# Kernel tuning notes

Hardware: AMD Instinct MI355X
Metric: run time of the kernel (lower is better)

Reference implementation:

```python
import jax, jax.numpy as jnp
import numpy as np

MIN_POS = 1e-6
EPS = 1e-20
B, S, F_IN, E, H = 2, 1024, 768, 768, 12
DH = E // H   # nnmf in_features per head (64)
FH = E // H   # nnmf out_features per head (hidden_features=embed_dim default)
N_NNMF_ITERS = 3
N_ALPHA_ITERS = 3


def l1norm(x, axis=-1):
    # F.normalize(x, p=1, dim=axis, eps=1e-20) for non-negative x
    return x / jnp.maximum(jnp.sum(jnp.abs(x), axis=axis, keepdims=True), EPS)


def setup_inputs() -> dict:
    key = jax.random.key(0)
    k = jax.random.split(key, 6)
    return {
        "x": jax.random.normal(k[0], (B, S, F_IN), jnp.float32),
        "embed_w": jax.random.normal(k[1], (E, F_IN), jnp.float32) * 0.02,
        "embed_b": jnp.zeros((E,), jnp.float32),
        "nnmf_w": jax.random.uniform(k[2], (FH, DH), jnp.float32),  # non-negative NMF dictionary
        "out_w": jax.random.normal(k[3], (F_IN, E), jnp.float32) * 0.02,
        "out_b": jnp.zeros((F_IN,), jnp.float32),
    }


def reference(x, embed_w, embed_b, nnmf_w, out_w, out_b):
    # normalize NMF weight rows (p=1 over in_features), as nnmf_layer.normalize_weights
    W = nnmf_w / jnp.maximum(jnp.sum(nnmf_w, axis=1, keepdims=True), EPS)  # [FH, DH]

    # embed + clamp positive, split heads
    xe = jnp.clip(x @ embed_w.T + embed_b, MIN_POS)            # [B,S,E]
    xe = xe.reshape(B, S, H, DH)                                # [B,S,H,DH]

    # NNMFDense: prepared_input = l1-normalized input (normalize_input_dim=-1)
    inp = l1norm(xe)                                            # [B,S,H,DH]
    h = l1norm(jnp.ones((B, S, H, FH), x.dtype))                # init hidden
    rec = inp
    for _ in range(N_NNMF_ITERS):
        rec = l1norm(jnp.clip(h @ W, MIN_POS))                  # reconstruction [B,S,H,DH]
        h = l1norm(jnp.clip(h * ((inp / rec) @ W.T), MIN_POS))  # multiplicative update

    # normalize_h (p=1, dim=-1)
    h = l1norm(h)                                               # [B,S,H,FH] -> 'bohf'

    # alpha dynamics fixed point
    alpha = jnp.ones((B, H, S, S), x.dtype)                     # 'bhoi'
    h_rec_input = rec * inp                                     # [B,S,H,DH]
    for _ in range(N_ALPHA_ITERS):
        h_mixed = jnp.einsum('bohf,bhoi->bihf', h, alpha)       # [B,S,H,FH]
        arec_inv = 1.0 / (h_mixed @ W + EPS)                    # _reconstruct -> [B,S,H,DH]
        alpha = alpha * jnp.einsum('bohf,bihf->bhoi', h_rec_input, arec_inv)

    out = jnp.einsum('bohf,bhoi->bihf', h, alpha)               # [B,S,H,FH]
    out = out.reshape(B, S, E)                                  # flatten heads
    return out @ out_w.T + out_b                                # out_project
```

## Files before the change

kernel.cpp:

```cpp
#include <hip/hip_runtime.h>

#define B_  2
#define S_  1024
#define FIN 768
#define E_  768
#define H_  12
#define DH  64

typedef unsigned int uint;
typedef unsigned short ushort;
typedef __attribute__((ext_vector_type(8))) short short8;
typedef __attribute__((ext_vector_type(4))) float floatx4;

__device__ __forceinline__ ushort f2bf(float f) {
    uint u = __float_as_uint(f);
    return (ushort)((u + 0x7fffu + ((u >> 16) & 1u)) >> 16);
}

__device__ __forceinline__ uint4 pack8(const ushort* p) {
    uint4 r;
    r.x = (uint)p[0] | ((uint)p[1] << 16);
    r.y = (uint)p[2] | ((uint)p[3] << 16);
    r.z = (uint)p[4] | ((uint)p[5] << 16);
    r.w = (uint)p[6] | ((uint)p[7] << 16);
    return r;
}

__device__ __forceinline__ void split8v(float4 a, float4 b, short8& hi, short8& lo) {
    float v[8] = {a.x, a.y, a.z, a.w, b.x, b.y, b.z, b.w};
    ushort h[8], l[8];
#pragma unroll
    for (int j = 0; j < 8; ++j) {
        h[j] = f2bf(v[j]);
        l[j] = f2bf(v[j] - __uint_as_float(((uint)h[j]) << 16));
    }
    uint4 H = pack8(h), L = pack8(l);
    hi = *(short8*)&H;
    lo = *(short8*)&L;
}

__global__ __launch_bounds__(256) void k_embed_prep(const float* __restrict__ xs,
                                                    const float* __restrict__ ew,
                                                    const float* __restrict__ eb,
                                                    const float* __restrict__ nw,
                                                    float* __restrict__ Wn,
                                                    float* __restrict__ WnT,
                                                    float* __restrict__ r1inv,
                                                    float* __restrict__ zbase,
                                                    float* __restrict__ inp) {
    __shared__ __align__(16) unsigned char smem[28160];
    const int tid = threadIdx.x;
    const int bid = blockIdx.x;

    if (bid >= 768) {
        const int pb = bid - 768;
        if (pb == 0) {
            float* Wl = (float*)smem;
            const int f = tid >> 2, q = tid & 3;
            float v[16];
            float s = 0.f;
#pragma unroll
            for (int i = 0; i < 16; ++i) { v[i] = nw[f * 64 + q * 16 + i]; s += v[i]; }
            s += __shfl_xor(s, 1, 64);
            s += __shfl_xor(s, 2, 64);
            const float inv = 1.f / fmaxf(s, 1e-20f);
#pragma unroll
            for (int i = 0; i < 16; ++i) {
                float w = v[i] * inv;
                Wn[f * 64 + q * 16 + i] = w;
                WnT[(q * 16 + i) * 64 + f] = w;
                Wl[f * 65 + q * 16 + i] = w;
            }
            __syncthreads();
            if (tid < 64) {
                float cs = 0.f;
                for (int ff = 0; ff < 64; ++ff) cs += Wl[ff * 65 + tid];
                float t = fmaxf(cs * (1.f / 64.f), 1e-6f);
                float S = t;
#pragma unroll
                for (int m = 1; m < 64; m <<= 1) S += __shfl_xor(S, m, 64);
                S = fmaxf(S, 1e-20f);
                r1inv[tid] = S / t;
            }
        } else {
            const int i = (pb - 1) * 1024 + tid * 4;
            if (i < 26112) {
                float4 z = make_float4(0.f, 0.f, 0.f, 0.f);
                *(float4*)(zbase + i) = z;
            }
        }
        return;
    }

    const int head = bid % 12;
    const int tok0 = (bid / 12) * 32;
    ushort* As_hi = (ushort*)smem;
    ushort* As_lo = As_hi + 32 * 72;
    ushort* Bs_hi = As_lo + 32 * 72;
    ushort* Bs_lo = Bs_hi + 64 * 72;
    float*  RS    = (float*)(Bs_lo + 64 * 72);

    const int wv = tid >> 6, lane = tid & 63;
    const int mbase = (wv >> 1) * 16;
    const int nbase = (wv & 1) * 32;
    const int lm = lane & 15, lq = lane >> 4;

    floatx4 acc[2];
    acc[0] = (floatx4)0.f;
    acc[1] = (floatx4)0.f;

    const int arow = tid >> 3, akc = (tid & 7) * 8;
    const int brow = tid >> 2, bkq = (tid & 3) * 16;
    const float* xrow = xs + (size_t)(tok0 + arow) * FIN + akc;
    const float* wrg  = ew + (size_t)(head * 64 + brow) * FIN + bkq;

    float4 pa[2], pb[4];
#pragma unroll
    for (int c = 0; c < 2; ++c) pa[c] = *(const float4*)(xrow + c * 4);
#pragma unroll
    for (int c = 0; c < 4; ++c) pb[c] = *(const float4*)(wrg + c * 4);

    for (int kb = 0; kb < FIN; kb += 64) {
        __syncthreads();
        {
            ushort ah[8], al[8], bh[16], bl[16];
            float va[8] = {pa[0].x, pa[0].y, pa[0].z, pa[0].w,
                           pa[1].x, pa[1].y, pa[1].z, pa[1].w};
#pragma unroll
            for (int j = 0; j < 8; ++j) {
                ah[j] = f2bf(va[j]);
                al[j] = f2bf(va[j] - __uint_as_float(((uint)ah[j]) << 16));
            }
#pragma unroll
            for (int c4 = 0; c4 < 4; ++c4) {
                float vb[4] = {pb[c4].x, pb[c4].y, pb[c4].z, pb[c4].w};
#pragma unroll
                for (int j = 0; j < 4; ++j) {
                    ushort g = f2bf(vb[j]);
                    bh[c4 * 4 + j] = g;
                    bl[c4 * 4 + j] = f2bf(vb[j] - __uint_as_float(((uint)g) << 16));
                }
            }
            const int aoff = arow * 72 + akc;
            *(uint4*)&As_hi[aoff] = pack8(ah);
            *(uint4*)&As_lo[aoff] = pack8(al);
            const int boff = brow * 72 + bkq;
            *(uint4*)&Bs_hi[boff]     = pack8(bh);
            *(uint4*)&Bs_hi[boff + 8] = pack8(bh + 8);
            *(uint4*)&Bs_lo[boff]     = pack8(bl);
            *(uint4*)&Bs_lo[boff + 8] = pack8(bl + 8);
        }
        __syncthreads();
        if (kb + 64 < FIN) {
#pragma unroll
            for (int c = 0; c < 2; ++c) pa[c] = *(const float4*)(xrow + kb + 64 + c * 4);
#pragma unroll
            for (int c = 0; c < 4; ++c) pb[c] = *(const float4*)(wrg + kb + 64 + c * 4);
        }
#pragma unroll
        for (int ch = 0; ch < 2; ++ch) {
            const int ko = ch * 32 + lq * 8;
            short8 ah = *(const short8*)&As_hi[(mbase + lm) * 72 + ko];
            short8 al = *(const short8*)&As_lo[(mbase + lm) * 72 + ko];
#pragma unroll
            for (int ti = 0; ti < 2; ++ti) {
                short8 bh = *(const short8*)&Bs_hi[(nbase + ti * 16 + lm) * 72 + ko];
                short8 bl = *(const short8*)&Bs_lo[(nbase + ti * 16 + lm) * 72 + ko];
                acc[ti] = __builtin_amdgcn_mfma_f32_16x16x32_bf16(ah, bh, acc[ti], 0, 0, 0);
                acc[ti] = __builtin_amdgcn_mfma_f32_16x16x32_bf16(al, bh, acc[ti], 0, 0, 0);
                acc[ti] = __builtin_amdgcn_mfma_f32_16x16x32_bf16(ah, bl, acc[ti], 0, 0, 0);
            }
        }
    }

    const float b0 = eb[head * 64 + nbase + lm];
    const float b1 = eb[head * 64 + nbase + 16 + lm];
    float xe[2][4];
    float rs[4];
#pragma unroll
    for (int r = 0; r < 4; ++r) {
        float e0 = fmaxf(acc[0][r] + b0, 1e-6f);
        float e1 = fmaxf(acc[1][r] + b1, 1e-6f);
        xe[0][r] = e0; xe[1][r] = e1;
        float p = e0 + e1;
        p += __shfl_xor(p, 1, 64);
        p += __shfl_xor(p, 2, 64);
        p += __shfl_xor(p, 4, 64);
        p += __shfl_xor(p, 8, 64);
        rs[r] = p;
    }
    if (lm == 0) {
#pragma unroll
        for (int r = 0; r < 4; ++r)
            RS[(wv & 1) * 32 + mbase + lq * 4 + r] = rs[r];
    }
    __syncthreads();
    const size_t obase = ((size_t)((tok0 >> 10) * 12 + head) * 1024 + (tok0 & 1023));
#pragma unroll
    for (int r = 0; r < 4; ++r) {
        const int m = mbase + lq * 4 + r;
        const float inv = 1.f / fmaxf(RS[m] + RS[32 + m], 1e-20f);
        float* op = inp + (obase + m) * 64;
        op[nbase + lm]      = xe[0][r] * inv;
        op[nbase + 16 + lm] = xe[1][r] * inv;
    }
}

__device__ __forceinline__ void mfma_matvec(const float srcC[4][4], float* T,
                                            int lm, int lq,
                                            const short8 Bh[4][2],
                                            const short8 Bl[4][2],
                                            floatx4 out[4]) {
#pragma unroll
    for (int nt = 0; nt < 4; ++nt)
#pragma unroll
        for (int r = 0; r < 4; ++r)
            T[(lq * 4 + r) * 68 + nt * 16 + lm] = srcC[nt][r];
    __syncthreads();
    float4 a00 = *(const float4*)&T[lm * 68 + lq * 8];
    float4 a01 = *(const float4*)&T[lm * 68 + lq * 8 + 4];
    float4 a10 = *(const float4*)&T[lm * 68 + 32 + lq * 8];
    float4 a11 = *(const float4*)&T[lm * 68 + 32 + lq * 8 + 4];
    short8 A0h, A0l, A1h, A1l;
    split8v(a00, a01, A0h, A0l);
    split8v(a10, a11, A1h, A1l);
#pragma unroll
    for (int nt = 0; nt < 4; ++nt) {
        floatx4 acc = (floatx4)0.f;
        acc = __builtin_amdgcn_mfma_f32_16x16x32_bf16(A0h, Bh[nt][0], acc, 0, 0, 0);
        acc = __builtin_amdgcn_mfma_f32_16x16x32_bf16(A0l, Bh[nt][0], acc, 0, 0, 0);
        acc = __builtin_amdgcn_mfma_f32_16x16x32_bf16(A0h, Bl[nt][0], acc, 0, 0, 0);
        acc = __builtin_amdgcn_mfma_f32_16x16x32_bf16(A1h, Bh[nt][1], acc, 0, 0, 0);
        acc = __builtin_amdgcn_mfma_f32_16x16x32_bf16(A1l, Bh[nt][1], acc, 0, 0, 0);
        acc = __builtin_amdgcn_mfma_f32_16x16x32_bf16(A1h, Bl[nt][1], acc, 0, 0, 0);
        out[nt] = acc;
    }
}

__global__ __launch_bounds__(256) void k_nnmf(const float* __restrict__ inp,
                                              const float* __restrict__ Wn,
                                              const float* __restrict__ WnT,
                                              const float* __restrict__ r1inv,
                                              float* __restrict__ hout,
                                              float* __restrict__ hriout,
                                              float* __restrict__ mp0) {
    __shared__ float Tb[4][16 * 68];
    const int tid = threadIdx.x, wv = tid >> 6, lane = tid & 63;
    const int lm = lane & 15, lq = lane >> 4;
    float* T = Tb[wv];
    const int rowbase = blockIdx.x * 64 + wv * 16;

    short8 Bt_h[4][2], Bt_l[4][2], Bw_h[4][2], Bw_l[4][2];
#pragma unroll
    for (int nt = 0; nt < 4; ++nt)
#pragma unroll
        for (int kc = 0; kc < 2; ++kc) {
            const int idx = (nt * 16 + lm) * 64 + kc * 32 + lq * 8;
            split8v(*(const float4*)(WnT + idx), *(const float4*)(WnT + idx + 4),
                    Bt_h[nt][kc], Bt_l[nt][kc]);
            split8v(*(const float4*)(Wn + idx), *(const float4*)(Wn + idx + 4),
                    Bw_h[nt][kc], Bw_l[nt][kc]);
        }

    float inpC[4][4];
#pragma unroll
    for (int nt = 0; nt < 4; ++nt)
#pragma unroll
        for (int r = 0; r < 4; ++r)
            inpC[nt][r] = inp[(size_t)(rowbase + lq * 4 + r) * 64 + nt * 16 + lm];
    float r1c[4];
#pragma unroll
    for (int nt = 0; nt < 4; ++nt) r1c[nt] = r1inv[nt * 16 + lm];

    float hC[4][4], recC[4][4];
    {
        float qC[4][4];
#pragma unroll
        for (int nt = 0; nt < 4; ++nt)
#pragma unroll
            for (int r = 0; r < 4; ++r) qC[nt][r] = inpC[nt][r] * r1c[nt];
        floatx4 u[4];
        mfma_matvec(qC, T, lm, lq, Bw_h, Bw_l, u);
#pragma unroll
        for (int nt = 0; nt < 4; ++nt)
#pragma unroll
            for (int r = 0; r < 4; ++r)
                hC[nt][r] = fmaxf(u[nt][r] * (1.f / 64.f), 1e-6f);
#pragma unroll
        for (int r = 0; r < 4; ++r) {
            float s = (hC[0][r] + hC[1][r]) + (hC[2][r] + hC[3][r]);
            s += __shfl_xor(s, 1, 64); s += __shfl_xor(s, 2, 64);
            s += __shfl_xor(s, 4, 64); s += __shfl_xor(s, 8, 64);
            const float inv = __builtin_amdgcn_rcpf(fmaxf(s, 1e-20f));
#pragma unroll
            for (int nt = 0; nt < 4; ++nt) hC[nt][r] *= inv;
        }
    }
#pragma unroll 1
    for (int it = 0; it < 2; ++it) {
        floatx4 t[4];
        mfma_matvec(hC, T, lm, lq, Bt_h, Bt_l, t);
        float tC[4][4], qC[4][4];
#pragma unroll
        for (int nt = 0; nt < 4; ++nt)
#pragma unroll
            for (int r = 0; r < 4; ++r) tC[nt][r] = fmaxf(t[nt][r], 1e-6f);
#pragma unroll
        for (int r = 0; r < 4; ++r) {
            float s = (tC[0][r] + tC[1][r]) + (tC[2][r] + tC[3][r]);
            s += __shfl_xor(s, 1, 64); s += __shfl_xor(s, 2, 64);
            s += __shfl_xor(s, 4, 64); s += __shfl_xor(s, 8, 64);
            s = fmaxf(s, 1e-20f);
            const float invS = __builtin_amdgcn_rcpf(s);
#pragma unroll
            for (int nt = 0; nt < 4; ++nt) {
                recC[nt][r] = tC[nt][r] * invS;
                qC[nt][r] = inpC[nt][r] * s * __builtin_amdgcn_rcpf(tC[nt][r]);
            }
        }
        floatx4 u[4];
        mfma_matvec(qC, T, lm, lq, Bw_h, Bw_l, u);
#pragma unroll
        for (int nt = 0; nt < 4; ++nt)
#pragma unroll
            for (int r = 0; r < 4; ++r)
                hC[nt][r] = fmaxf(hC[nt][r] * u[nt][r], 1e-6f);
#pragma unroll
        for (int r = 0; r < 4; ++r) {
            float s = (hC[0][r] + hC[1][r]) + (hC[2][r] + hC[3][r]);
            s += __shfl_xor(s, 1, 64); s += __shfl_xor(s, 2, 64);
            s += __shfl_xor(s, 4, 64); s += __shfl_xor(s, 8, 64);
            const float inv = __builtin_amdgcn_rcpf(fmaxf(s, 1e-20f));
#pragma unroll
            for (int nt = 0; nt < 4; ++nt) hC[nt][r] *= inv;
        }
    }
#pragma unroll
    for (int r = 0; r < 4; ++r) {
        float s = (hC[0][r] + hC[1][r]) + (hC[2][r] + hC[3][r]);
        s += __shfl_xor(s, 1, 64); s += __shfl_xor(s, 2, 64);
        s += __shfl_xor(s, 4, 64); s += __shfl_xor(s, 8, 64);
        const float inv = __builtin_amdgcn_rcpf(fmaxf(s, 1e-20f));
#pragma unroll
        for (int nt = 0; nt < 4; ++nt) hC[nt][r] *= inv;
    }
#pragma unroll
    for (int nt = 0; nt < 4; ++nt)
#pragma unroll
        for (int r = 0; r < 4; ++r) {
            const size_t o = (size_t)(rowbase + lq * 4 + r) * 64 + nt * 16 + lm;
            hout[o] = hC[nt][r];
            hriout[o] = recC[nt][r] * inpC[nt][r];
        }
    float hs[4];
#pragma unroll
    for (int nt = 0; nt < 4; ++nt) {
        float s = (hC[nt][0] + hC[nt][1]) + (hC[nt][2] + hC[nt][3]);
        s += __shfl_xor(s, 16, 64);
        s += __shfl_xor(s, 32, 64);
        hs[nt] = s;
    }
    float mvv = lq == 0 ? hs[0] : lq == 1 ? hs[1] : lq == 2 ? hs[2] : hs[3];
    atomicAdd(&mp0[(size_t)blockIdx.x * 64 + lq * 16 + lm], mvv);
}

__global__ __launch_bounds__(256) void k_alpha_step(const float* __restrict__ hin,
                                                    const float* __restrict__ hri,
                                                    const float* __restrict__ Wn,
                                                    const float* __restrict__ mp_in,
                                                    float* __restrict__ mp_out,
                                                    float* __restrict__ c,
                                                    float* __restrict__ M,
                                                    int it) {
    __shared__ float mred[4][64];
    __shared__ float mv[64];
    __shared__ float vv[64];
    __shared__ float cl[64];
    const int tid = threadIdx.x;
    const int bh = blockIdx.x >> 4;
    const int chunk = blockIdx.x & 15;
    const size_t rowbase = (size_t)bh * 1024 + chunk * 64;

    {
        int f = tid & 63, p = tid >> 6;
        float s = 0.f;
#pragma unroll
        for (int pp = 0; pp < 4; ++pp)
            s += mp_in[((size_t)bh * 16 + p * 4 + pp) * 64 + f];
        mred[p][f] = s;
    }
    __syncthreads();
    if (tid < 64)
        mv[tid] = (mred[0][tid] + mred[1][tid]) + (mred[2][tid] + mred[3][tid]);
    __syncthreads();
    {
        int d = tid & 63, qq = tid >> 6;
        float r = 0.f;
#pragma unroll
        for (int ff = 0; ff < 16; ++ff)
            r = fmaf(mv[qq * 16 + ff], Wn[(size_t)(qq * 16 + ff) * 64 + d], r);
        mred[qq][d] = r;
    }
    __syncthreads();
    if (tid < 64)
        vv[tid] = 1.f / (((mred[0][tid] + mred[1][tid]) + (mred[2][tid] + mred[3][tid])) + 1e-20f);
    __syncthreads();
    {
        int o = tid >> 2, dq = tid & 3;
        const float* rp = hri + (rowbase + o) * 64 + dq * 16;
        float dot = 0.f;
#pragma unroll
        for (int t4 = 0; t4 < 16; t4 += 4) {
            float4 r4 = *(const float4*)(rp + t4);
            dot = fmaf(r4.x, vv[dq * 16 + t4 + 0], dot);
            dot = fmaf(r4.y, vv[dq * 16 + t4 + 1], dot);
            dot = fmaf(r4.z, vv[dq * 16 + t4 + 2], dot);
            dot = fmaf(r4.w, vv[dq * 16 + t4 + 3], dot);
        }
        dot += __shfl_xor(dot, 1, 64);
        dot += __shfl_xor(dot, 2, 64);
        float cn = dot;
        if (it >= 2) cn *= c[rowbase + o];
        if (dq == 0) { c[rowbase + o] = cn; cl[o] = cn; }
    }
    __syncthreads();
    {
        const int f4 = (tid & 15) * 4, ogr = tid >> 4;
        float4 a = make_float4(0.f, 0.f, 0.f, 0.f);
#pragma unroll
        for (int oi = 0; oi < 4; ++oi) {
            int o = ogr * 4 + oi;
            float4 h4 = *(const float4*)(hin + (rowbase + o) * 64 + f4);
            float cv = cl[o];
            a.x = fmaf(h4.x, cv, a.x); a.y = fmaf(h4.y, cv, a.y);
            a.z = fmaf(h4.z, cv, a.z); a.w = fmaf(h4.w, cv, a.w);
        }
        a.x += __shfl_xor(a.x, 16, 64); a.y += __shfl_xor(a.y, 16, 64);
        a.z += __shfl_xor(a.z, 16, 64); a.w += __shfl_xor(a.w, 16, 64);
        a.x += __shfl_xor(a.x, 32, 64); a.y += __shfl_xor(a.y, 32, 64);
        a.z += __shfl_xor(a.z, 32, 64); a.w += __shfl_xor(a.w, 32, 64);
        const int w = tid >> 6;
        if ((tid & 63) < 16) *(float4*)&mred[w][(tid & 15) * 4] = a;
    }
    __syncthreads();
    if (tid < 64) {
        float s = (mred[0][tid] + mred[1][tid]) + (mred[2][tid] + mred[3][tid]);
        if (it == 3) atomicAdd(&M[(size_t)bh * 64 + tid], s);
        else mp_out[((size_t)bh * 16 + chunk) * 64 + tid] = s;
    }
}

__global__ __launch_bounds__(256) void k_projbcast(const float* __restrict__ M,
                                                   const float* __restrict__ ow,
                                                   const float* __restrict__ ob,
                                                   float* __restrict__ out) {
    __shared__ float Ml[768];
    __shared__ float ps[4][64];
    __shared__ float yseg[64];
    const int tid = threadIdx.x;
    const int b = blockIdx.x / 192;
    const int rem = blockIdx.x - b * 192;
    const int jt = rem >> 4, rg = rem & 15;
    for (int i = tid; i < 768; i += 256) Ml[i] = M[b * 768 + i];
    __syncthreads();
    const int jj = tid & 63, part = tid >> 6;
    const int j = jt * 64 + jj;
    const float* row = ow + (size_t)j * 768 + part * 192;
    float acc = 0.f;
    for (int t = 0; t < 192; t += 4) {
        float4 w4 = *(const float4*)(row + t);
        acc = fmaf(w4.x, Ml[part * 192 + t + 0], acc);
        acc = fmaf(w4.y, Ml[part * 192 + t + 1], acc);
        acc = fmaf(w4.z, Ml[part * 192 + t + 2], acc);
        acc = fmaf(w4.w, Ml[part * 192 + t + 3], acc);
    }
    ps[part][jj] = acc;
    __syncthreads();
    if (tid < 64)
        yseg[tid] = ps[0][tid] + ps[1][tid] + ps[2][tid] + ps[3][tid] + ob[jt * 64 + tid];
    __syncthreads();
    const int r0 = tid >> 2, c4 = (tid & 3) * 16;
    float4 v4[4];
#pragma unroll
    for (int q = 0; q < 4; ++q) v4[q] = *(const float4*)&yseg[c4 + q * 4];
    float* dst = out + ((size_t)(b * 1024 + rg * 64 + r0)) * 768 + jt * 64 + c4;
#pragma unroll
    for (int q = 0; q < 4; ++q) *(float4*)(dst + q * 4) = v4[q];
}

extern "C" void kernel_launch(void* const* d_in, const int* in_sizes, int n_in,
                              void* d_out, int out_size, void* d_ws, size_t ws_size,
                              hipStream_t stream) {
    const float* xs = (const float*)d_in[0];
    const float* ew = (const float*)d_in[1];
    const float* eb = (const float*)d_in[2];
    const float* nw = (const float*)d_in[3];
    const float* ow = (const float*)d_in[4];
    const float* ob = (const float*)d_in[5];
    float* out = (float*)d_out;

    float* ws    = (float*)d_ws;
    float* inp   = ws;
    float* h     = ws + 1572864;
    float* hri   = ws + 3145728;
    float* Wn    = ws + 4718592;
    float* WnT   = ws + 4722688;
    float* r1inv = ws + 4726784;
    float* mp0   = ws + 4727040;
    float* M     = ws + 4751616;
    float* mp1   = ws + 4753152;
    float* mp2   = ws + 4777728;
    float* c     = ws + 4802304;

    k_embed_prep<<<795, 256, 0, stream>>>(xs, ew, eb, nw, Wn, WnT, r1inv, mp0, inp);
    k_nnmf<<<384, 256, 0, stream>>>(inp, Wn, WnT, r1inv, h, hri, mp0);
    k_alpha_step<<<384, 256, 0, stream>>>(h, hri, Wn, mp0, mp1, c, M, 1);
    k_alpha_step<<<384, 256, 0, stream>>>(h, hri, Wn, mp1, mp2, c, M, 2);
    k_alpha_step<<<384, 256, 0, stream>>>(h, hri, Wn, mp2, mp1, c, M, 3);
    k_projbcast<<<384, 256, 0, stream>>>(M, ow, ob, out);
}
```

Before: 137.9 us.

## Halve embed GEMM token tile to double block count; use wave barriers in matvec

The embed+normalize kernel now processes 16 tokens per block instead of 32, with each of the 4 waves computing a 16x16 output tile. This doubles the grid to 1536 compute blocks for better CU occupancy, at the cost of reloading the weight tile twice as often. Separately, the per-wave transpose in mfma_matvec replaces a block-wide __syncthreads with wave-level barriers, since each wave uses its own scratch region. That removes cross-wave stalls but is only correct if T is private to each wave.

```diff
diff --git a/kernel.cpp b/kernel.cpp
--- a/kernel.cpp
+++ b/kernel.cpp
@@ -48,12 +48,12 @@
                                                     float* __restrict__ r1inv,
                                                     float* __restrict__ zbase,
                                                     float* __restrict__ inp) {
-    __shared__ __align__(16) unsigned char smem[28160];
+    __shared__ __align__(16) unsigned char smem[23360];
     const int tid = threadIdx.x;
     const int bid = blockIdx.x;
 
-    if (bid >= 768) {
-        const int pb = bid - 768;
+    if (bid >= 1536) {
+        const int pb = bid - 1536;
         if (pb == 0) {
             float* Wl = (float*)smem;
             const int f = tid >> 2, q = tid & 3;
@@ -93,44 +93,48 @@
     }
 
     const int head = bid % 12;
-    const int tok0 = (bid / 12) * 32;
+    const int tok0 = (bid / 12) * 16;
     ushort* As_hi = (ushort*)smem;
-    ushort* As_lo = As_hi + 32 * 72;
-    ushort* Bs_hi = As_lo + 32 * 72;
+    ushort* As_lo = As_hi + 16 * 72;
+    ushort* Bs_hi = As_lo + 16 * 72;
     ushort* Bs_lo = Bs_hi + 64 * 72;
     float*  RS    = (float*)(Bs_lo + 64 * 72);
 
     const int wv = tid >> 6, lane = tid & 63;
-    const int mbase = (wv >> 1) * 16;
-    const int nbase = (wv & 1) * 32;
+    const int nbase = wv * 16;
     const int lm = lane & 15, lq = lane >> 4;
 
-    floatx4 acc[2];
-    acc[0] = (floatx4)0.f;
-    acc[1] = (floatx4)0.f;
-
-    const int arow = tid >> 3, akc = (tid & 7) * 8;
+    floatx4 acc = (floatx4)0.f;
+
+    const int arow = tid >> 4, akc = (tid & 15) * 4;
     const int brow = tid >> 2, bkq = (tid & 3) * 16;
     const float* xrow = xs + (size_t)(tok0 + arow) * FIN + akc;
     const float* wrg  = ew + (size_t)(head * 64 + brow) * FIN + bkq;
 
-    float4 pa[2], pb[4];
-#pragma unroll
-    for (int c = 0; c < 2; ++c) pa[c] = *(const float4*)(xrow + c * 4);
+    float4 pa, pb[4];
+    pa = *(const float4*)(xrow);
 #pragma unroll
     for (int c = 0; c < 4; ++c) pb[c] = *(const float4*)(wrg + c * 4);
 
     for (int kb = 0; kb < FIN; kb += 64) {
         __syncthreads();
         {
-            ushort ah[8], al[8], bh[16], bl[16];
-            float va[8] = {pa[0].x, pa[0].y, pa[0].z, pa[0].w,
-                           pa[1].x, pa[1].y, pa[1].z, pa[1].w};
-#pragma unroll
-            for (int j = 0; j < 8; ++j) {
+            float va[4] = {pa.x, pa.y, pa.z, pa.w};
+            ushort ah[4], al[4];
+#pragma unroll
+            for (int j = 0; j < 4; ++j) {
                 ah[j] = f2bf(va[j]);
                 al[j] = f2bf(va[j] - __uint_as_float(((uint)ah[j]) << 16));
             }
+            uint2 pAh, pAl;
+            pAh.x = (uint)ah[0] | ((uint)ah[1] << 16);
+            pAh.y = (uint)ah[2] | ((uint)ah[3] << 16);
+            pAl.x = (uint)al[0] | ((uint)al[1] << 16);
+            pAl.y = (uint)al[2] | ((uint)al[3] << 16);
+            *(uint2*)&As_hi[arow * 72 + akc] = pAh;
+            *(uint2*)&As_lo[arow * 72 + akc] = pAl;
+
+            ushort bh[16], bl[16];
 #pragma unroll
             for (int c4 = 0; c4 < 4; ++c4) {
                 float vb[4] = {pb[c4].x, pb[c4].y, pb[c4].z, pb[c4].w};
@@ -141,9 +145,6 @@
                     bl[c4 * 4 + j] = f2bf(vb[j] - __uint_as_float(((uint)g) << 16));
                 }
             }
-            const int aoff = arow * 72 + akc;
-            *(uint4*)&As_hi[aoff] = pack8(ah);
-            *(uint4*)&As_lo[aoff] = pack8(al);
             const int boff = brow * 72 + bkq;
             *(uint4*)&Bs_hi[boff]     = pack8(bh);
             *(uint4*)&Bs_hi[boff + 8] = pack8(bh + 8);
@@ -152,37 +153,31 @@
         }
         __syncthreads();
         if (kb + 64 < FIN) {
-#pragma unroll
-            for (int c = 0; c < 2; ++c) pa[c] = *(const float4*)(xrow + kb + 64 + c * 4);
+            pa = *(const float4*)(xrow + kb + 64);
 #pragma unroll
             for (int c = 0; c < 4; ++c) pb[c] = *(const float4*)(wrg + kb + 64 + c * 4);
         }
 #pragma unroll
         for (int ch = 0; ch < 2; ++ch) {
             const int ko = ch * 32 + lq * 8;
-            short8 ah = *(const short8*)&As_hi[(mbase + lm) * 72 + ko];
-            short8 al = *(const short8*)&As_lo[(mbase + lm) * 72 + ko];
-#pragma unroll
-            for (int ti = 0; ti < 2; ++ti) {
-                short8 bh = *(const short8*)&Bs_hi[(nbase + ti * 16 + lm) * 72 + ko];
-                short8 bl = *(const short8*)&Bs_lo[(nbase + ti * 16 + lm) * 72 + ko];
-                acc[ti] = __builtin_amdgcn_mfma_f32_16x16x32_bf16(ah, bh, acc[ti], 0, 0, 0);
-                acc[ti] = __builtin_amdgcn_mfma_f32_16x16x32_bf16(al, bh, acc[ti], 0, 0, 0);
-                acc[ti] = __builtin_amdgcn_mfma_f32_16x16x32_bf16(ah, bl, acc[ti], 0, 0, 0);
-            }
+            short8 ah = *(const short8*)&As_hi[lm * 72 + ko];
+            short8 al = *(const short8*)&As_lo[lm * 72 + ko];
+            short8 bh = *(const short8*)&Bs_hi[(nbase + lm) * 72 + ko];
+            short8 bl = *(const short8*)&Bs_lo[(nbase + lm) * 72 + ko];
+            acc = __builtin_amdgcn_mfma_f32_16x16x32_bf16(ah, bh, acc, 0, 0, 0);
+            acc = __builtin_amdgcn_mfma_f32_16x16x32_bf16(al, bh, acc, 0, 0, 0);
+            acc = __builtin_amdgcn_mfma_f32_16x16x32_bf16(ah, bl, acc, 0, 0, 0);
         }
     }
 
     const float b0 = eb[head * 64 + nbase + lm];
-    const float b1 = eb[head * 64 + nbase + 16 + lm];
-    float xe[2][4];
+    float xe[4];
     float rs[4];
 #pragma unroll
     for (int r = 0; r < 4; ++r) {
-        float e0 = fmaxf(acc[0][r] + b0, 1e-6f);
-        float e1 = fmaxf(acc[1][r] + b1, 1e-6f);
-        xe[0][r] = e0; xe[1][r] = e1;
-        float p = e0 + e1;
+        float e = fmaxf(acc[r] + b0, 1e-6f);
+        xe[r] = e;
+        float p = e;
         p += __shfl_xor(p, 1, 64);
         p += __shfl_xor(p, 2, 64);
         p += __shfl_xor(p, 4, 64);
@@ -191,18 +186,16 @@
     }
     if (lm == 0) {
 #pragma unroll
-        for (int r = 0; r < 4; ++r)
-            RS[(wv & 1) * 32 + mbase + lq * 4 + r] = rs[r];
+        for (int r = 0; r < 4; ++r) RS[wv * 16 + lq * 4 + r] = rs[r];
     }
     __syncthreads();
     const size_t obase = ((size_t)((tok0 >> 10) * 12 + head) * 1024 + (tok0 & 1023));
 #pragma unroll
     for (int r = 0; r < 4; ++r) {
-        const int m = mbase + lq * 4 + r;
-        const float inv = 1.f / fmaxf(RS[m] + RS[32 + m], 1e-20f);
-        float* op = inp + (obase + m) * 64;
-        op[nbase + lm]      = xe[0][r] * inv;
-        op[nbase + 16 + lm] = xe[1][r] * inv;
+        const int m = lq * 4 + r;
+        const float tot = RS[m] + RS[16 + m] + RS[32 + m] + RS[48 + m];
+        const float inv = 1.f / fmaxf(tot, 1e-20f);
+        inp[(obase + m) * 64 + nbase + lm] = xe[r] * inv;
     }
 }
 
@@ -211,16 +204,18 @@
                                             const short8 Bh[4][2],
                                             const short8 Bl[4][2],
                                             floatx4 out[4]) {
+    __builtin_amdgcn_wave_barrier();
 #pragma unroll
     for (int nt = 0; nt < 4; ++nt)
 #pragma unroll
         for (int r = 0; r < 4; ++r)
             T[(lq * 4 + r) * 68 + nt * 16 + lm] = srcC[nt][r];
-    __syncthreads();
+    __builtin_amdgcn_wave_barrier();
     float4 a00 = *(const float4*)&T[lm * 68 + lq * 8];
     float4 a01 = *(const float4*)&T[lm * 68 + lq * 8 + 4];
     float4 a10 = *(const float4*)&T[lm * 68 + 32 + lq * 8];
     float4 a11 = *(const float4*)&T[lm * 68 + 32 + lq * 8 + 4];
+    __builtin_amdgcn_wave_barrier();
     short8 A0h, A0l, A1h, A1l;
     split8v(a00, a01, A0h, A0l);
     split8v(a10, a11, A1h, A1l);
@@ -512,7 +507,7 @@
     float* mp2   = ws + 4777728;
     float* c     = ws + 4802304;
 
-    k_embed_prep<<<795, 256, 0, stream>>>(xs, ew, eb, nw, Wn, WnT, r1inv, mp0, inp);
+    k_embed_prep<<<1563, 256, 0, stream>>>(xs, ew, eb, nw, Wn, WnT, r1inv, mp0, inp);
     k_nnmf<<<384, 256, 0, stream>>>(inp, Wn, WnT, r1inv, h, hri, mp0);
     k_alpha_step<<<384, 256, 0, stream>>>(h, hri, Wn, mp0, mp1, c, M, 1);
     k_alpha_step<<<384, 256, 0, stream>>>(h, hri, Wn, mp1, mp2, c, M, 2);
```

Result: slower. 144.3 us (+4.7%).
